# Optimization experiments

Hardware: AMD Instinct MI355X
Metric: run time of the kernel (lower is better)

Reference implementation:

```python
import jax, jax.numpy as jnp
import numpy as np


def setup_inputs() -> dict:
    key = jax.random.key(0)
    k1, k2 = jax.random.split(key)
    N, H, W, C = 8, 512, 512, 32
    image = jax.random.normal(k1, (N, H, W, C), dtype=jnp.float32)
    flow = jax.random.normal(k2, (N, H, W, 2), dtype=jnp.float32)
    return {"image": image, "flow": flow}


def dense_image_warp(image, flow):
    """Faithful port of tfa.image.dense_image_warp with bilinear interp.

    query_points = grid - flow; floor clamped to [0, size-2]; alpha in [0,1].
    """
    N, H, W, C = image.shape
    dt = flow.dtype
    gy, gx = jnp.meshgrid(jnp.arange(H, dtype=dt), jnp.arange(W, dtype=dt), indexing="ij")
    qy = gy[None] - flow[..., 0]  # (N,H,W)
    qx = gx[None] - flow[..., 1]
    fy_f = jnp.clip(jnp.floor(qy), 0.0, H - 2)
    fx_f = jnp.clip(jnp.floor(qx), 0.0, W - 2)
    ay = jnp.clip(qy - fy_f, 0.0, 1.0)[..., None]  # (N,H,W,1)
    ax = jnp.clip(qx - fx_f, 0.0, 1.0)[..., None]
    fy = fy_f.astype(jnp.int32)
    fx = fx_f.astype(jnp.int32)
    b = jnp.arange(N)[:, None, None]
    tl = image[b, fy, fx]          # (N,H,W,C)
    tr = image[b, fy, fx + 1]
    bl = image[b, fy + 1, fx]
    br = image[b, fy + 1, fx + 1]
    top = tl + ax * (tr - tl)
    bot = bl + ax * (br - bl)
    return top + ay * (bot - top)


def reference(image, flow):
    return dense_image_warp(image, flow)
```

## Files before the change

kernel.cpp:

```cpp
#include <hip/hip_runtime.h>


#define C_CH   32
#define C4_CH  8

__global__ __launch_bounds__(256) void dense_warp_kernel(
    const float* __restrict__ image,
    const float* __restrict__ flow,
    float* __restrict__ out,
    int H, int W, int total_threads) {
  int tid = blockIdx.x * blockDim.x + threadIdx.x;
  if (tid >= total_threads) return;

  int c4  = tid & (C4_CH - 1);
  int pix = tid >> 3;
  int w   = pix & (W - 1);
  int nh  = pix >> 9;
  int h   = nh & (H - 1);

  float2 fl = ((const float2*)flow)[pix];
  float qy = (float)h - fl.x;
  float qx = (float)w - fl.y;

  float fy_f = fminf(fmaxf(floorf(qy), 0.0f), (float)(H - 2));
  float fx_f = fminf(fmaxf(floorf(qx), 0.0f), (float)(W - 2));
  float ay = fminf(fmaxf(qy - fy_f, 0.0f), 1.0f);
  float ax = fminf(fmaxf(qx - fx_f, 0.0f), 1.0f);
  int fy = (int)fy_f;
  int fx = (int)fx_f;

  const float4* img4 = (const float4*)image;
  int n_base = (pix >> 18) * (H * W);
  int row0 = (n_base + ((h - h)  + 0)) ;
  (void)row0;
  int idx_tl = ((n_base + fy * W + fx) << 3) + c4;
  int idx_tr = idx_tl + C4_CH;
  int idx_bl = idx_tl + (W << 3);
  int idx_br = idx_bl + C4_CH;

  float4 tl = img4[idx_tl];
  float4 tr = img4[idx_tr];
  float4 bl = img4[idx_bl];
  float4 br = img4[idx_br];

  float4 r;
  {
    float top = tl.x + ax * (tr.x - tl.x);
    float bot = bl.x + ax * (br.x - bl.x);
    r.x = top + ay * (bot - top);
  }
  {
    float top = tl.y + ax * (tr.y - tl.y);
    float bot = bl.y + ax * (br.y - bl.y);
    r.y = top + ay * (bot - top);
  }
  {
    float top = tl.z + ax * (tr.z - tl.z);
    float bot = bl.z + ax * (br.z - bl.z);
    r.z = top + ay * (bot - top);
  }
  {
    float top = tl.w + ax * (tr.w - tl.w);
    float bot = bl.w + ax * (br.w - bl.w);
    r.w = top + ay * (bot - top);
  }

  ((float4*)out)[tid] = r;
}

extern "C" void kernel_launch(void* const* d_in, const int* in_sizes, int n_in,
                              void* d_out, int out_size, void* d_ws, size_t ws_size,
                              hipStream_t stream) {
  const float* image = (const float*)d_in[0];
  const float* flow  = (const float*)d_in[1];
  float* out = (float*)d_out;

  const int N = 8, H = 512, W = 512;
  int total = N * H * W * C4_CH;
  int block = 256;
  int grid = (total + block - 1) / block;
  dense_warp_kernel<<<grid, block, 0, stream>>>(image, flow, out, H, W, total);
}
```

Measured before the change: 437.3 us.

## Process two pixels per thread, swizzle blocks across XCDs, use nontemporal stores

Each thread now handles two pixels 32 apart, issuing eight gathered float4 loads together to raise memory-level parallelism, and the grid is halved. Block IDs are remapped so that consecutive blocks dispatched round-robin to the 8 XCDs cover contiguous image regions per XCD, which is meant to improve L2 locality for the gathered neighbours. Output writes use nontemporal stores so they do not pollute the cache. Shapes are hardcoded, and the change adds register pressure.

```diff
diff --git a/kernel.cpp b/kernel.cpp
--- a/kernel.cpp
+++ b/kernel.cpp
@@ -1,71 +1,77 @@
 #include <hip/hip_runtime.h>
 
 
-#define C_CH   32
-#define C4_CH  8
+typedef float f4 __attribute__((ext_vector_type(4)));
+
+#define C4_CH 8
 
 __global__ __launch_bounds__(256) void dense_warp_kernel(
     const float* __restrict__ image,
     const float* __restrict__ flow,
-    float* __restrict__ out,
-    int H, int W, int total_threads) {
-  int tid = blockIdx.x * blockDim.x + threadIdx.x;
-  if (tid >= total_threads) return;
+    float* __restrict__ out) {
+  const int H = 512, W = 512;
 
-  int c4  = tid & (C4_CH - 1);
-  int pix = tid >> 3;
-  int w   = pix & (W - 1);
-  int nh  = pix >> 9;
-  int h   = nh & (H - 1);
+  int bid = blockIdx.x;
+  int swz = (bid & 7) * 4096 + (bid >> 3);
 
-  float2 fl = ((const float2*)flow)[pix];
-  float qy = (float)h - fl.x;
-  float qx = (float)w - fl.y;
+  int t  = threadIdx.x;
+  int c4 = t & (C4_CH - 1);
+  int lp = t >> 3;
 
-  float fy_f = fminf(fmaxf(floorf(qy), 0.0f), (float)(H - 2));
-  float fx_f = fminf(fmaxf(floorf(qx), 0.0f), (float)(W - 2));
-  float ay = fminf(fmaxf(qy - fy_f, 0.0f), 1.0f);
-  float ax = fminf(fmaxf(qx - fx_f, 0.0f), 1.0f);
-  int fy = (int)fy_f;
-  int fx = (int)fx_f;
+  int pixbase = swz << 6;
+  int p0 = pixbase + lp;
+  int p1 = p0 + 32;
 
-  const float4* img4 = (const float4*)image;
-  int n_base = (pix >> 18) * (H * W);
-  int row0 = (n_base + ((h - h)  + 0)) ;
-  (void)row0;
-  int idx_tl = ((n_base + fy * W + fx) << 3) + c4;
-  int idx_tr = idx_tl + C4_CH;
-  int idx_bl = idx_tl + (W << 3);
-  int idx_br = idx_bl + C4_CH;
+  const float2* fl2 = (const float2*)flow;
+  float2 f0 = fl2[p0];
+  float2 f1 = fl2[p1];
 
-  float4 tl = img4[idx_tl];
-  float4 tr = img4[idx_tr];
-  float4 bl = img4[idx_bl];
-  float4 br = img4[idx_br];
+  int w0 = p0 & (W - 1);
+  int h0 = (p0 >> 9) & (H - 1);
+  int w1 = p1 & (W - 1);
+  int h1 = (p1 >> 9) & (H - 1);
+  int nb0 = (p0 >> 18) << 18;
+  int nb1 = (p1 >> 18) << 18;
 
-  float4 r;
-  {
-    float top = tl.x + ax * (tr.x - tl.x);
-    float bot = bl.x + ax * (br.x - bl.x);
-    r.x = top + ay * (bot - top);
-  }
-  {
-    float top = tl.y + ax * (tr.y - tl.y);
-    float bot = bl.y + ax * (br.y - bl.y);
-    r.y = top + ay * (bot - top);
-  }
-  {
-    float top = tl.z + ax * (tr.z - tl.z);
-    float bot = bl.z + ax * (br.z - bl.z);
-    r.z = top + ay * (bot - top);
-  }
-  {
-    float top = tl.w + ax * (tr.w - tl.w);
-    float bot = bl.w + ax * (br.w - bl.w);
-    r.w = top + ay * (bot - top);
-  }
+  float qy0 = (float)h0 - f0.x, qx0 = (float)w0 - f0.y;
+  float qy1 = (float)h1 - f1.x, qx1 = (float)w1 - f1.y;
 
-  ((float4*)out)[tid] = r;
+  float fy0f = fminf(fmaxf(floorf(qy0), 0.0f), (float)(H - 2));
+  float fx0f = fminf(fmaxf(floorf(qx0), 0.0f), (float)(W - 2));
+  float fy1f = fminf(fmaxf(floorf(qy1), 0.0f), (float)(H - 2));
+  float fx1f = fminf(fmaxf(floorf(qx1), 0.0f), (float)(W - 2));
+  float ay0 = fminf(fmaxf(qy0 - fy0f, 0.0f), 1.0f);
+  float ax0 = fminf(fmaxf(qx0 - fx0f, 0.0f), 1.0f);
+  float ay1 = fminf(fmaxf(qy1 - fy1f, 0.0f), 1.0f);
+  float ax1 = fminf(fmaxf(qx1 - fx1f, 0.0f), 1.0f);
+  int fy0 = (int)fy0f, fx0 = (int)fx0f;
+  int fy1 = (int)fy1f, fx1 = (int)fx1f;
+
+  const f4* img4 = (const f4*)image;
+  int i0 = ((nb0 + fy0 * W + fx0) << 3) + c4;
+  int i1 = ((nb1 + fy1 * W + fx1) << 3) + c4;
+  const int rowstep = W << 3;
+
+  f4 tl0 = img4[i0];
+  f4 tr0 = img4[i0 + C4_CH];
+  f4 bl0 = img4[i0 + rowstep];
+  f4 br0 = img4[i0 + rowstep + C4_CH];
+  f4 tl1 = img4[i1];
+  f4 tr1 = img4[i1 + C4_CH];
+  f4 bl1 = img4[i1 + rowstep];
+  f4 br1 = img4[i1 + rowstep + C4_CH];
+
+  f4 top0 = tl0 + ax0 * (tr0 - tl0);
+  f4 bot0 = bl0 + ax0 * (br0 - bl0);
+  f4 r0   = top0 + ay0 * (bot0 - top0);
+
+  f4 top1 = tl1 + ax1 * (tr1 - tl1);
+  f4 bot1 = bl1 + ax1 * (br1 - bl1);
+  f4 r1   = top1 + ay1 * (bot1 - top1);
+
+  f4* out4 = (f4*)out;
+  __builtin_nontemporal_store(r0, &out4[(p0 << 3) + c4]);
+  __builtin_nontemporal_store(r1, &out4[(p1 << 3) + c4]);
 }
 
 extern "C" void kernel_launch(void* const* d_in, const int* in_sizes, int n_in,
@@ -75,9 +81,5 @@
   const float* flow  = (const float*)d_in[1];
   float* out = (float*)d_out;
 
-  const int N = 8, H = 512, W = 512;
-  int total = N * H * W * C4_CH;
-  int block = 256;
-  int grid = (total + block - 1) / block;
-  dense_warp_kernel<<<grid, block, 0, stream>>>(image, flow, out, H, W, total);
+  dense_warp_kernel<<<32768, 256, 0, stream>>>(image, flow, out);
 }
```

Result: slower. 449.5 us (+2.8%).
